# Kernel optimization log

Measured on AMD Instinct MI355X. Metric: run time of the kernel, lower is better.

## Reference

```python
import jax, jax.numpy as jnp
import numpy as np

B, D, T, NT, DS, G = 1024, 512, 36, 64, 32, 4
EPS = 1e-5


def setup_inputs() -> dict:
    key = jax.random.key(0)
    ks = jax.random.split(key, 8)
    return {
        "x": jax.random.normal(ks[0], (B, D, T, 1), jnp.float32),
        "y": jax.random.normal(ks[1], (B, D, T, 1), jnp.float32),
        "my_tokens": jax.random.normal(ks[2], (NT, D), jnp.float32) * 0.02,
        "gate": jax.random.normal(ks[3], (1,), jnp.float32) * 0.1,
        "gate_av": jax.random.normal(ks[4], (1,), jnp.float32) * 0.1,
        "w_down": jax.random.normal(ks[5], (DS, D // G), jnp.float32) * 0.05,  # Conv2d(512->32,1,groups=4) weight [32,128,1,1] squeezed
        "w_up": jax.random.normal(ks[6], (D, DS // G), jnp.float32) * 0.05,    # Conv2d(32->512,1,groups=4) weight [512,8,1,1] squeezed
        "bn1_g": jnp.ones((DS,), jnp.float32), "bn1_b": jnp.zeros((DS,), jnp.float32),
        "bn2_g": jnp.ones((D,), jnp.float32), "bn2_b": jnp.zeros((D,), jnp.float32),
        "lnb_g": jnp.ones((D,), jnp.float32), "lnb_b": jnp.zeros((D,), jnp.float32),
        "lnp_g": jnp.ones((D,), jnp.float32), "lnp_b": jnp.zeros((D,), jnp.float32),
    }


def _layernorm(h, g, b):  # normalize last dim
    mu = jnp.mean(h, axis=-1, keepdims=True)
    var = jnp.var(h, axis=-1, keepdims=True)
    return (h - mu) * jax.lax.rsqrt(var + EPS) * g + b


def _batchnorm(z, g, b):  # z: [B,C,T], training-mode batch stats over (B,T)
    mu = jnp.mean(z, axis=(0, 2), keepdims=True)
    var = jnp.var(z, axis=(0, 2), keepdims=True)
    return (z - mu) * jax.lax.rsqrt(var + EPS) * g[None, :, None] + b[None, :, None]


def reference(x, y, my_tokens, gate, gate_av, w_down, w_up,
              bn1_g, bn1_b, bn2_g, bn2_b, lnb_g, lnb_b, lnp_g, lnp_b):
    xs = x[..., 0]  # [B,D,T]
    ys = y[..., 0]  # [B,D,T]
    # token <- y cross attention
    att_y2tk = jax.nn.softmax(jnp.einsum('td,bds->bts', my_tokens, ys), axis=-1)  # [B,NT,T]
    rep = my_tokens[None] + jnp.einsum('bts,bds->btd', att_y2tk, ys)  # [B,NT,D]
    # x <- token cross attention
    att_tk2x = jax.nn.softmax(jnp.einsum('bds,btd->bst', xs, rep), axis=-1)  # [B,T,NT]
    x_res = jnp.einsum('bst,btd->bsd', att_tk2x, rep)  # [B,T,D]
    xc = xs + gate_av[0] * jnp.swapaxes(x_res, 1, 2)  # [B,D,T]
    # ln_before over channel dim
    h = jnp.swapaxes(_layernorm(jnp.swapaxes(xc, 1, 2), lnb_g, lnb_b), 1, 2)  # [B,D,T]
    # grouped 1x1 down conv
    hg = h.reshape(h.shape[0], G, D // G, T)
    z = jnp.einsum('bgct,goc->bgot', hg, w_down.reshape(G, DS // G, D // G)).reshape(h.shape[0], DS, T)
    z = jax.nn.relu(_batchnorm(z, bn1_g, bn1_b))
    # grouped 1x1 up conv
    zg = z.reshape(z.shape[0], G, DS // G, T)
    o = jnp.einsum('bgct,goc->bgot', zg, w_up.reshape(G, D // G, DS // G)).reshape(z.shape[0], D, T)
    o = _batchnorm(o, bn2_g, bn2_b)
    o = jnp.swapaxes(_layernorm(jnp.swapaxes(o, 1, 2), lnp_g, lnp_b), 1, 2)
    return (gate[0] * o)[..., None]  # [B,D,T,1]
```

## Files before the change

### kernel.cpp

```cpp
#include <hip/hip_runtime.h>

#define B_ 1024
#define D_ 512
#define T_ 36
#define NT_ 64
#define DS_ 32
#define EPS_ 1e-5f

typedef float f32x4 __attribute__((ext_vector_type(4)));
typedef __bf16 bf16x8 __attribute__((ext_vector_type(8)));
typedef unsigned short u16x8 __attribute__((ext_vector_type(8)));

#define DEVI static __device__ __forceinline__
#define MFMA16 __builtin_amdgcn_mfma_f32_16x16x32_bf16

DEVI unsigned short f2bf(float f) { return __builtin_bit_cast(unsigned short, (__bf16)f); }
DEVI float bf2f(unsigned short h) { return (float)__builtin_bit_cast(__bf16, h); }

DEVI unsigned swz(int row, int col) {
    return (unsigned)(row * 1024 + ((2 * col) ^ ((row & 7) << 4)));
}

#define OFF_XST 73728
#define OFF_SC  122880
#define OFF_A1  133632
#define OFF_A2  142848
#define OFF_GT  149760
#define K1_LDS  156672

__global__ __launch_bounds__(512)
void k0_prepack(const float* __restrict__ tok, const float* __restrict__ wd,
                unsigned short* __restrict__ tokbf, float* __restrict__ tokTf,
                unsigned short* __restrict__ wdd)
{
    int i = blockIdx.x * 512 + threadIdx.x;
    if (i < 32768) {
        tokbf[i] = f2bf(tok[i]);
    } else if (i < 65536) {
        int j = i - 32768; int d = j >> 6, t = j & 63;
        tokTf[j] = tok[t * 512 + d];
    } else if (i < 81920) {
        int j = i - 65536; int o = j >> 9, dd = j & 511;
        wdd[j] = ((dd >> 7) == (o >> 3)) ? f2bf(wd[o * 128 + (dd & 127)]) : (unsigned short)0;
    }
}

__global__ __launch_bounds__(1024, 4)
void k1_fused(const float* __restrict__ x, const float* __restrict__ y,
              const unsigned short* __restrict__ tokbf, const float* __restrict__ tokTf,
              const float* __restrict__ gav_p, const unsigned short* __restrict__ wdd,
              const float* __restrict__ lnbg, const float* __restrict__ lnbb,
              float* __restrict__ z_pre)
{
    extern __shared__ char lds[];
    float* sc = (float*)(lds + OFF_SC);
    unsigned short* a1 = (unsigned short*)(lds + OFF_A1);
    unsigned short* a2 = (unsigned short*)(lds + OFF_A2);
    unsigned short* gt = (unsigned short*)(lds + OFF_GT);

    const int b    = blockIdx.x;
    const int tid  = threadIdx.x;
    const int lane = tid & 63;
    const int w    = tid >> 6;
    const int l15  = lane & 15;
    const int l4   = lane >> 4;

    const float* yb = y + b * (D_ * T_);
    const float* xb = x + b * (D_ * T_);

    {
        unsigned* z1 = (unsigned*)(lds + 36 * 1024);
        unsigned* z2 = (unsigned*)(lds + OFF_XST + 36 * 1024);
        for (int i = tid; i < 3072; i += 1024) { z1[i] = 0u; z2[i] = 0u; }
        unsigned* z3 = (unsigned*)(lds + OFF_A1);
        for (int i = tid; i < 5760; i += 1024) z3[i] = 0u;
    }
    for (int ww = tid; ww < 1152; ww += 1024) {
        int isx = (ww >= 576) ? 1 : 0;
        int u = isx ? (ww - 576) : ww;
        const float* src = isx ? xb : yb;
        char* dst = lds + (isx ? OFF_XST : 0);
        int dblk = u / 9, s4 = u - dblk * 9;
        int s0 = s4 * 4;
        const float* bp = src + dblk * 8 * T_ + s0;
        u16x8 u0, u1, u2, u3;
        #pragma unroll
        for (int r = 0; r < 8; ++r) {
            f32x4 v = *(const f32x4*)(bp + r * T_);
            u0[r] = f2bf(v[0]); u1[r] = f2bf(v[1]);
            u2[r] = f2bf(v[2]); u3[r] = f2bf(v[3]);
        }
        *(u16x8*)(dst + swz(s0 + 0, dblk * 8)) = u0;
        *(u16x8*)(dst + swz(s0 + 1, dblk * 8)) = u1;
        *(u16x8*)(dst + swz(s0 + 2, dblk * 8)) = u2;
        *(u16x8*)(dst + swz(s0 + 3, dblk * 8)) = u3;
    }
    __syncthreads();

    for (int tile = w; tile < 21; tile += 16) {
        f32x4 acc0 = {0.f,0.f,0.f,0.f}, acc1 = {0.f,0.f,0.f,0.f};
        if (tile < 12) {
            int mt = tile / 3, nt = tile % 3;
            int trow = mt * 16 + l15, srow = nt * 16 + l15;
            #pragma unroll
            for (int ks = 0; ks < 16; ks += 2) {
                int ka = ks * 32 + l4 * 8, kb = ka + 32;
                acc0 = MFMA16(*(const bf16x8*)(tokbf + trow * 512 + ka),
                              *(const bf16x8*)(lds + swz(srow, ka)), acc0, 0, 0, 0);
                acc1 = MFMA16(*(const bf16x8*)(tokbf + trow * 512 + kb),
                              *(const bf16x8*)(lds + swz(srow, kb)), acc1, 0, 0, 0);
            }
            f32x4 acc = acc0 + acc1;
            if (srow < T_) {
                #pragma unroll
                for (int j = 0; j < 4; ++j)
                    sc[(mt * 16 + l4 * 4 + j) * 42 + srow] = acc[j];
            }
        } else {
            int g2 = tile - 12;
            int mt = g2 / 3, nt = g2 % 3;
            int arow = mt * 16 + l15, brow = nt * 16 + l15;
            #pragma unroll
            for (int ks = 0; ks < 16; ks += 2) {
                int ka = ks * 32 + l4 * 8, kb = ka + 32;
                acc0 = MFMA16(*(const bf16x8*)(lds + OFF_XST + swz(arow, ka)),
                              *(const bf16x8*)(lds + swz(brow, ka)), acc0, 0, 0, 0);
                acc1 = MFMA16(*(const bf16x8*)(lds + OFF_XST + swz(arow, kb)),
                              *(const bf16x8*)(lds + swz(brow, kb)), acc1, 0, 0, 0);
            }
            f32x4 acc = acc0 + acc1;
            if (brow < T_) {
                #pragma unroll
                for (int j = 0; j < 4; ++j) {
                    int gr = mt * 16 + l4 * 4 + j;
                    if (gr < T_) gt[gr * 72 + brow] = f2bf(acc[j]);
                }
            }
        }
    }
    __syncthreads();

    {
        int t = tid >> 4, l16 = tid & 15;
        const float* scp = sc + t * 42;
        float v0 = scp[l16];
        float v1 = scp[l16 + 16];
        float v2 = (l16 < 4) ? scp[l16 + 32] : -1e30f;
        float m = fmaxf(fmaxf(v0, v1), v2);
        #pragma unroll
        for (int off = 1; off < 16; off <<= 1) m = fmaxf(m, __shfl_xor(m, off));
        float e0 = __expf(v0 - m), e1 = __expf(v1 - m);
        float e2 = (l16 < 4) ? __expf(v2 - m) : 0.f;
        float ssum = e0 + e1 + e2;
        #pragma unroll
        for (int off = 1; off < 16; off <<= 1) ssum += __shfl_xor(ssum, off);
        float inv = 1.f / ssum;
        a1[t * 72 + l16]      = f2bf(e0 * inv);
        a1[t * 72 + l16 + 16] = f2bf(e1 * inv);
        if (l16 < 4) a1[t * 72 + l16 + 32] = f2bf(e2 * inv);
    }
    __syncthreads();

    #pragma unroll
    for (int i = 0; i < 8; ++i) {
        int q = w + 16 * i;
        int dt = q & 31, tt = q >> 5;
        int dbase = dt * 16, tbase = tt * 16;
        const float* yrow = yb + (dbase + l15) * T_;
        f32x4 p0 = *(const f32x4*)(yrow + l4 * 8);
        f32x4 p1 = *(const f32x4*)(yrow + l4 * 8 + 4);
        bf16x8 fa0, fa1;
        #pragma unroll
        for (int j = 0; j < 4; ++j) { fa0[j] = (__bf16)p0[j]; fa0[4 + j] = (__bf16)p1[j]; }
        if (l4 == 0) {
            f32x4 p2 = *(const f32x4*)(yrow + 32);
            #pragma unroll
            for (int j = 0; j < 4; ++j) { fa1[j] = (__bf16)p2[j]; fa1[4 + j] = (__bf16)0.f; }
        } else {
            #pragma unroll
            for (int j = 0; j < 8; ++j) fa1[j] = (__bf16)0.f;
        }
        bf16x8 fb0 = *(const bf16x8*)(a1 + (tbase + l15) * 72 + l4 * 8);
        bf16x8 fb1 = *(const bf16x8*)(a1 + (tbase + l15) * 72 + 32 + l4 * 8);
        f32x4 acc = {0.f,0.f,0.f,0.f};
        acc = MFMA16(fa0, fb0, acc, 0, 0, 0);
        acc = MFMA16(fa1, fb1, acc, 0, 0, 0);
        #pragma unroll
        for (int j = 0; j < 4; ++j) {
            int d = dbase + l4 * 4 + j;
            float val = tokTf[d * 64 + tbase + l15] + acc[j];
            *(unsigned short*)(lds + d * 144 + 2 * (tbase + l15)) = f2bf(val);
        }
    }
    if (w < 12) {
        int mt = w / 3, nt = w % 3;
        int trow = mt * 16 + l15, srow = nt * 16 + l15;
        f32x4 acc0 = {0.f,0.f,0.f,0.f}, acc1 = {0.f,0.f,0.f,0.f};
        #pragma unroll
        for (int ks = 0; ks < 16; ks += 2) {
            int ka = ks * 32 + l4 * 8, kb = ka + 32;
            acc0 = MFMA16(*(const bf16x8*)(tokbf + trow * 512 + ka),
                          *(const bf16x8*)(lds + OFF_XST + swz(srow, ka)), acc0, 0, 0, 0);
            acc1 = MFMA16(*(const bf16x8*)(tokbf + trow * 512 + kb),
                          *(const bf16x8*)(lds + OFF_XST + swz(srow, kb)), acc1, 0, 0, 0);
        }
        acc0 = MFMA16(*(const bf16x8*)(a1 + trow * 72 + l4 * 8),
                      *(const bf16x8*)(gt + srow * 72 + l4 * 8), acc0, 0, 0, 0);
        acc1 = MFMA16(*(const bf16x8*)(a1 + trow * 72 + 32 + l4 * 8),
                      *(const bf16x8*)(gt + srow * 72 + 32 + l4 * 8), acc1, 0, 0, 0);
        f32x4 acc = acc0 + acc1;
        if (srow < T_) {
            #pragma unroll
            for (int j = 0; j < 4; ++j)
                sc[(mt * 16 + l4 * 4 + j) * 42 + srow] = acc[j];
        }
    }
    __syncthreads();

    if (tid < 576) {
        int s = tid >> 4, l16 = tid & 15;
        float v0 = sc[(l16     ) * 42 + s];
        float v1 = sc[(l16 + 16) * 42 + s];
        float v2 = sc[(l16 + 32) * 42 + s];
        float v3 = sc[(l16 + 48) * 42 + s];
        float m = fmaxf(fmaxf(v0, v1), fmaxf(v2, v3));
        #pragma unroll
        for (int off = 1; off < 16; off <<= 1) m = fmaxf(m, __shfl_xor(m, off));
        float e0 = __expf(v0 - m), e1 = __expf(v1 - m), e2 = __expf(v2 - m), e3 = __expf(v3 - m);
        float ssum = e0 + e1 + e2 + e3;
        #pragma unroll
        for (int off = 1; off < 16; off <<= 1) ssum += __shfl_xor(ssum, off);
        float inv = 1.f / ssum;
        a2[s * 72 + l16]      = f2bf(e0 * inv);
        a2[s * 72 + l16 + 16] = f2bf(e1 * inv);
        a2[s * 72 + l16 + 32] = f2bf(e2 * inv);
        a2[s * 72 + l16 + 48] = f2bf(e3 * inv);
    }
    __syncthreads();

    {
        const float gav = gav_p[0];
        float* red = sc;
        f32x4 acc6[6];
        #pragma unroll
        for (int i = 0; i < 6; ++i) {
            int q = w * 6 + i;
            int dt = q & 31, st = q >> 5;
            int dbase = dt * 16, sbase = st * 16;
            f32x4 acc = {0.f,0.f,0.f,0.f};
            #pragma unroll
            for (int ks = 0; ks < 2; ++ks) {
                int k0 = ks * 32 + l4 * 8;
                bf16x8 af = *(const bf16x8*)(lds + (dbase + l15) * 144 + k0 * 2);
                bf16x8 bv = *(const bf16x8*)(a2 + (sbase + l15) * 72 + k0);
                acc = MFMA16(af, bv, acc, 0, 0, 0);
            }
            acc6[i] = acc;
        }
        #pragma unroll
        for (int i = 0; i < 6; ++i) {
            int q = w * 6 + i;
            int dt = q & 31, st = q >> 5;
            int dbase = dt * 16, sbase = st * 16;
            int s = sbase + l15;
            float rsum = 0.f, rsq = 0.f;
            if (s < T_) {
                #pragma unroll
                for (int j = 0; j < 4; ++j) {
                    int d = dbase + l4 * 4 + j;
                    float xsv = bf2f(*(const unsigned short*)(lds + OFF_XST + swz(s, d)));
                    float v = xsv + gav * acc6[i][j];
                    acc6[i][j] = v;
                    rsum += v; rsq += v * v;
                }
            }
            rsum += __shfl_xor(rsum, 16); rsq += __shfl_xor(rsq, 16);
            rsum += __shfl_xor(rsum, 32); rsq += __shfl_xor(rsq, 32);
            if (s < T_ && l4 == 0) {
                red[s * 32 + dt] = rsum;
                red[1152 + s * 32 + dt] = rsq;
            }
        }
        __syncthreads();
        if (tid < T_) {
            int s = tid; float S = 0.f, Q = 0.f;
            #pragma unroll
            for (int q = 0; q < 32; ++q) { S += red[s * 32 + q]; Q += red[1152 + s * 32 + q]; }
            float mu = S * (1.f / 512.f);
            float var = Q * (1.f / 512.f) - mu * mu;
            red[2304 + s] = mu; red[2340 + s] = rsqrtf(var + EPS_);
        }
        __syncthreads();
        #pragma unroll
        for (int i = 0; i < 6; ++i) {
            int q = w * 6 + i;
            int dt = q & 31, st = q >> 5;
            int dbase = dt * 16, sbase = st * 16;
            int s = sbase + l15;
            if (s < T_) {
                float mu = red[2304 + s], rsig = red[2340 + s];
                #pragma unroll
                for (int j = 0; j < 4; ++j) {
                    int d = dbase + l4 * 4 + j;
                    float g = lnbg[d], bb2 = lnbb[d];
                    *(unsigned short*)(lds + OFF_XST + swz(s, d)) =
                        f2bf((acc6[i][j] - mu) * rsig * g + bb2);
                }
            }
        }
    }
    __syncthreads();

    if (w < 6) {
        int mt = w / 3, nt = w % 3;
        int orow = mt * 16 + l15, srow = nt * 16 + l15;
        f32x4 acc0 = {0.f,0.f,0.f,0.f}, acc1 = {0.f,0.f,0.f,0.f};
        #pragma unroll
        for (int ks = 0; ks < 16; ks += 2) {
            int ka = ks * 32 + l4 * 8, kb = ka + 32;
            acc0 = MFMA16(*(const bf16x8*)(wdd + orow * 512 + ka),
                          *(const bf16x8*)(lds + OFF_XST + swz(srow, ka)), acc0, 0, 0, 0);
            acc1 = MFMA16(*(const bf16x8*)(wdd + orow * 512 + kb),
                          *(const bf16x8*)(lds + OFF_XST + swz(srow, kb)), acc1, 0, 0, 0);
        }
        f32x4 acc = acc0 + acc1;
        if (srow < T_) {
            #pragma unroll
            for (int j = 0; j < 4; ++j)
                z_pre[b * (DS_ * T_) + (mt * 16 + l4 * 4 + j) * T_ + srow] = acc[j];
        }
    }
}

__global__ __launch_bounds__(256)
void k3a_bn1part(const float* __restrict__ z_pre, float* __restrict__ p3)
{
    __shared__ float rbuf[4][2];
    int blk = blockIdx.x;
    int o = blk & 31, sl = blk >> 5;
    int tid = threadIdx.x;
    float S = 0.f, Q = 0.f;
    for (int i = tid; i < 64 * T_; i += 256) {
        int bb = sl * 64 + i / T_, t = i - (i / T_) * T_;
        float v = z_pre[bb * (DS_ * T_) + o * T_ + t];
        S += v; Q += v * v;
    }
    #pragma unroll
    for (int off = 1; off < 64; off <<= 1) { S += __shfl_xor(S, off); Q += __shfl_xor(Q, off); }
    int ww = tid >> 6;
    if ((tid & 63) == 0) { rbuf[ww][0] = S; rbuf[ww][1] = Q; }
    __syncthreads();
    if (tid == 0) {
        float s2 = 0.f, q2 = 0.f;
        for (int i = 0; i < 4; ++i) { s2 += rbuf[i][0]; q2 += rbuf[i][1]; }
        p3[blk * 2] = s2; p3[blk * 2 + 1] = q2;
    }
}

__global__ __launch_bounds__(64)
void k3b_bn1stats(const float* __restrict__ p3, float* __restrict__ st1)
{
    int o = threadIdx.x;
    if (o < 32) {
        float S = 0.f, Q = 0.f;
        for (int sl = 0; sl < 16; ++sl) {
            S += p3[((sl << 5) | o) * 2];
            Q += p3[((sl << 5) | o) * 2 + 1];
        }
        float mu = S / 36864.f;
        float var = Q / 36864.f - mu * mu;
        st1[o] = mu; st1[32 + o] = rsqrtf(var + EPS_);
    }
}

__global__ __launch_bounds__(256)
void k4m_moments(const float* __restrict__ z_pre, const float* __restrict__ st1,
                 const float* __restrict__ g1p, const float* __restrict__ b1p,
                 float* __restrict__ m4)
{
    __shared__ float zr[32][40];
    int blk = blockIdx.x, tid = threadIdx.x;
    int c2 = tid & 7, c1 = (tid >> 3) & 7, g = tid >> 6;
    int ch1 = g * 8 + c1, ch2 = g * 8 + c2;
    float acc = 0.f, asum = 0.f;
    for (int bi = 0; bi < 8; ++bi) {
        int b = blk * 8 + bi;
        __syncthreads();
        for (int i = tid; i < DS_ * T_; i += 256) {
            int o = i / T_, t = i - o * T_;
            float v = z_pre[b * (DS_ * T_) + i];
            zr[o][t] = fmaxf(0.f, (v - st1[o]) * st1[32 + o] * g1p[o] + b1p[o]);
        }
        __syncthreads();
        for (int t = 0; t < T_; ++t) {
            float a = zr[ch1][t], b2 = zr[ch2][t];
            acc += a * b2;
            asum += a;
        }
    }
    m4[blk * 288 + tid] = acc;
    if (c1 == c2) m4[blk * 288 + 256 + g * 8 + c1] = asum;
}

__global__ __launch_bounds__(512)
void k4s_bn2stats(const float* __restrict__ m4, const float* __restrict__ wu,
                  float* __restrict__ st2)
{
    __shared__ float M2[256], mz[32];
    int tid = threadIdx.x;
    if (tid < 256) {
        float S = 0.f;
        for (int k = 0; k < 128; ++k) S += m4[k * 288 + tid];
        M2[tid] = S * (1.f / 36864.f);
    } else if (tid < 288) {
        int j = tid - 256;
        float S = 0.f;
        for (int k = 0; k < 128; ++k) S += m4[k * 288 + 256 + j];
        mz[j] = S * (1.f / 36864.f);
    }
    __syncthreads();
    int d = tid, g = d >> 7;
    float wr[8];
    #pragma unroll
    for (int c = 0; c < 8; ++c) wr[c] = wu[d * 8 + c];
    float mu2 = 0.f;
    #pragma unroll
    for (int c = 0; c < 8; ++c) mu2 += wr[c] * mz[g * 8 + c];
    float e2 = 0.f;
    #pragma unroll
    for (int c = 0; c < 8; ++c)
        #pragma unroll
        for (int c2 = 0; c2 < 8; ++c2)
            e2 += wr[c] * wr[c2] * M2[g * 64 + c * 8 + c2];
    st2[d] = mu2;
    st2[512 + d] = rsqrtf(e2 - mu2 * mu2 + EPS_);
}

#define K5_LDS 47888
__global__ __launch_bounds__(512, 6)
void k5_final(const float* __restrict__ z_pre, const float* __restrict__ st1,
              const float* __restrict__ g1p, const float* __restrict__ b1p,
              const float* __restrict__ wu, const float* __restrict__ st2,
              const float* __restrict__ g2p, const float* __restrict__ b2p,
              const float* __restrict__ lnpg, const float* __restrict__ lnpb,
              const float* __restrict__ gate_p, float* __restrict__ out)
{
    extern __shared__ char lds[];
    unsigned short* o_f = (unsigned short*)lds;
    float* zrT = (float*)(lds + 41984);
    int b = blockIdx.x;
    int tid = threadIdx.x;

    for (int i = tid; i < DS_ * T_; i += 512) {
        int o = i / T_, s = i - o * T_;
        float v = z_pre[b * (DS_ * T_) + i];
        zrT[s * 41 + o] = fmaxf(0.f, (v - st1[o]) * st1[32 + o] * g1p[o] + b1p[o]);
    }
    __syncthreads();

    for (int i = tid; i < D_ * T_; i += 512) {
        int d = i / T_, t = i - d * T_;
        const float* zp = &zrT[t * 41 + (d >> 7) * 8];
        const float* wp = &wu[d * 8];
        f32x4 w0 = *(const f32x4*)wp;
        f32x4 w1 = *(const f32x4*)(wp + 4);
        float acc = zp[0]*w0[0] + zp[1]*w0[1] + zp[2]*w0[2] + zp[3]*w0[3]
                  + zp[4]*w1[0] + zp[5]*w1[1] + zp[6]*w1[2] + zp[7]*w1[3];
        o_f[d * 41 + t] = f2bf((acc - st2[d]) * st2[512 + d] * g2p[d] + b2p[d]);
    }
    __syncthreads();

    int w = tid >> 6, lane = tid & 63;
    float gate = gate_p[0];
    for (int t = w; t < T_; t += 8) {
        float S = 0.f, Q = 0.f;
        float v[8];
        #pragma unroll
        for (int i2 = 0; i2 < 8; ++i2) {
            float vv = bf2f(o_f[(i2 * 64 + lane) * 41 + t]);
            v[i2] = vv; S += vv; Q += vv * vv;
        }
        #pragma unroll
        for (int off = 1; off < 64; off <<= 1) { S += __shfl_xor(S, off); Q += __shfl_xor(Q, off); }
        float mu = S * (1.f / 512.f);
        float var = Q * (1.f / 512.f) - mu * mu;
        float rs = rsqrtf(var + EPS_);
        #pragma unroll
        for (int i2 = 0; i2 < 8; ++i2) {
            int d = i2 * 64 + lane;
            o_f[d * 41 + t] = f2bf(gate * ((v[i2] - mu) * rs * lnpg[d] + lnpb[d]));
        }
    }
    __syncthreads();

    float* ob = out + b * (D_ * T_);
    for (int i = tid; i < D_ * T_; i += 512) {
        int d = i / T_, t = i - d * T_;
        ob[i] = bf2f(o_f[d * 41 + t]);
    }
}

extern "C" void kernel_launch(void* const* d_in, const int* in_sizes, int n_in,
                              void* d_out, int out_size, void* d_ws, size_t ws_size,
                              hipStream_t stream)
{
    (void)in_sizes; (void)n_in; (void)out_size; (void)ws_size;
    const float* x    = (const float*)d_in[0];
    const float* y    = (const float*)d_in[1];
    const float* tok  = (const float*)d_in[2];
    const float* gate = (const float*)d_in[3];
    const float* gav  = (const float*)d_in[4];
    const float* wd   = (const float*)d_in[5];
    const float* wu   = (const float*)d_in[6];
    const float* bn1g = (const float*)d_in[7];
    const float* bn1b = (const float*)d_in[8];
    const float* bn2g = (const float*)d_in[9];
    const float* bn2b = (const float*)d_in[10];
    const float* lnbg = (const float*)d_in[11];
    const float* lnbb = (const float*)d_in[12];
    const float* lnpg = (const float*)d_in[13];
    const float* lnpb = (const float*)d_in[14];
    float* out = (float*)d_out;

    char* ws = (char*)d_ws;
    float* z_pre          = (float*)ws;
    float* st1            = (float*)(ws + 4718592);
    unsigned short* tokbf = (unsigned short*)(ws + 4719104);
    float* tokTf          = (float*)(ws + 4784640);
    unsigned short* wdd   = (unsigned short*)(ws + 4915712);
    float* p3             = (float*)(ws + 4948480);
    float* m4             = (float*)(ws + 4952576);
    float* st2            = (float*)(ws + 5100032);

    hipFuncSetAttribute((const void*)k1_fused, hipFuncAttributeMaxDynamicSharedMemorySize, K1_LDS);
    hipFuncSetAttribute((const void*)k5_final, hipFuncAttributeMaxDynamicSharedMemorySize, K5_LDS);

    k0_prepack<<<160, 512, 0, stream>>>(tok, wd, tokbf, tokTf, wdd);
    k1_fused<<<B_, 1024, K1_LDS, stream>>>(x, y, tokbf, tokTf, gav, wdd, lnbg, lnbb, z_pre);
    k3a_bn1part<<<512, 256, 0, stream>>>(z_pre, p3);
    k3b_bn1stats<<<1, 64, 0, stream>>>(p3, st1);
    k4m_moments<<<128, 256, 0, stream>>>(z_pre, st1, bn1g, bn1b, m4);
    k4s_bn2stats<<<1, 512, 0, stream>>>(m4, wu, st2);
    k5_final<<<B_, 512, K5_LDS, stream>>>(z_pre, st1, bn1g, bn1b, wu, st2, bn2g, bn2b,
                                          lnpg, lnpb, gate, out);
}
```

Baseline: 212.9 us.

## Stage y as bf16 in LDS and reuse A fragments across token tiles

```diff
diff --git a/kernel.cpp b/kernel.cpp
--- a/kernel.cpp
+++ b/kernel.cpp
@@ -10,6 +10,7 @@
 typedef float f32x4 __attribute__((ext_vector_type(4)));
 typedef __bf16 bf16x8 __attribute__((ext_vector_type(8)));
 typedef unsigned short u16x8 __attribute__((ext_vector_type(8)));
+typedef unsigned short u16x4 __attribute__((ext_vector_type(4)));
 
 #define DEVI static __device__ __forceinline__
 #define MFMA16 __builtin_amdgcn_mfma_f32_16x16x32_bf16
@@ -159,37 +160,51 @@
         a1[t * 72 + l16 + 16] = f2bf(e1 * inv);
         if (l16 < 4) a1[t * 72 + l16 + 32] = f2bf(e2 * inv);
     }
-    __syncthreads();
-
-    #pragma unroll
-    for (int i = 0; i < 8; ++i) {
-        int q = w + 16 * i;
-        int dt = q & 31, tt = q >> 5;
-        int dbase = dt * 16, tbase = tt * 16;
-        const float* yrow = yb + (dbase + l15) * T_;
-        f32x4 p0 = *(const f32x4*)(yrow + l4 * 8);
-        f32x4 p1 = *(const f32x4*)(yrow + l4 * 8 + 4);
-        bf16x8 fa0, fa1;
-        #pragma unroll
-        for (int j = 0; j < 4; ++j) { fa0[j] = (__bf16)p0[j]; fa0[4 + j] = (__bf16)p1[j]; }
-        if (l4 == 0) {
-            f32x4 p2 = *(const f32x4*)(yrow + 32);
-            #pragma unroll
-            for (int j = 0; j < 4; ++j) { fa1[j] = (__bf16)p2[j]; fa1[4 + j] = (__bf16)0.f; }
-        } else {
-            #pragma unroll
-            for (int j = 0; j < 8; ++j) fa1[j] = (__bf16)0.f;
-        }
-        bf16x8 fb0 = *(const bf16x8*)(a1 + (tbase + l15) * 72 + l4 * 8);
-        bf16x8 fb1 = *(const bf16x8*)(a1 + (tbase + l15) * 72 + 32 + l4 * 8);
-        f32x4 acc = {0.f,0.f,0.f,0.f};
-        acc = MFMA16(fa0, fb0, acc, 0, 0, 0);
-        acc = MFMA16(fa1, fb1, acc, 0, 0, 0);
-        #pragma unroll
-        for (int j = 0; j < 4; ++j) {
-            int d = dbase + l4 * 4 + j;
-            float val = tokTf[d * 64 + tbase + l15] + acc[j];
-            *(unsigned short*)(lds + d * 144 + 2 * (tbase + l15)) = f2bf(val);
+    for (int j = tid; j < 4608; j += 1024) {
+        int row = j / 9, q = j - row * 9;
+        f32x4 v = *(const f32x4*)(yb + row * 36 + q * 4);
+        u16x4 h;
+        #pragma unroll
+        for (int jj = 0; jj < 4; ++jj) h[jj] = f2bf(v[jj]);
+        *(u16x4*)(lds + row * 144 + q * 8) = h;
+    }
+    if (tid < 512) {
+        char* p = lds + tid * 144;
+        u16x4 z4 = {0,0,0,0}; u16x8 z8 = {0,0,0,0,0,0,0,0};
+        *(u16x4*)(p + 72) = z4;
+        *(u16x8*)(p + 80) = z8;
+        *(u16x8*)(p + 96) = z8;
+        *(u16x8*)(p + 112) = z8;
+    }
+    __syncthreads();
+
+    {
+        #pragma unroll
+        for (int half = 0; half < 2; ++half) {
+            int dbase = (w + 16 * half) * 16;
+            bf16x8 fa0 = *(const bf16x8*)(lds + (dbase + l15) * 144 + l4 * 16);
+            bf16x8 fa1 = *(const bf16x8*)(lds + (dbase + l15) * 144 + 64 + l4 * 16);
+            f32x4 c[4];
+            #pragma unroll
+            for (int tt = 0; tt < 4; ++tt) {
+                int tbase = tt * 16;
+                bf16x8 fb0 = *(const bf16x8*)(a1 + (tbase + l15) * 72 + l4 * 8);
+                bf16x8 fb1 = *(const bf16x8*)(a1 + (tbase + l15) * 72 + 32 + l4 * 8);
+                f32x4 acc = {0.f,0.f,0.f,0.f};
+                acc = MFMA16(fa0, fb0, acc, 0, 0, 0);
+                acc = MFMA16(fa1, fb1, acc, 0, 0, 0);
+                c[tt] = acc;
+            }
+            #pragma unroll
+            for (int tt = 0; tt < 4; ++tt) {
+                int tbase = tt * 16;
+                #pragma unroll
+                for (int j = 0; j < 4; ++j) {
+                    int d = dbase + l4 * 4 + j;
+                    float val = tokTf[d * 64 + tbase + l15] + c[tt][j];
+                    *(unsigned short*)(lds + d * 144 + 2 * (tbase + l15)) = f2bf(val);
+                }
+            }
         }
     }
     if (w < 12) {
@@ -277,18 +292,18 @@
             rsum += __shfl_xor(rsum, 16); rsq += __shfl_xor(rsq, 16);
             rsum += __shfl_xor(rsum, 32); rsq += __shfl_xor(rsq, 32);
             if (s < T_ && l4 == 0) {
-                red[s * 32 + dt] = rsum;
-                red[1152 + s * 32 + dt] = rsq;
+                red[dt * 40 + s] = rsum;
+                red[1280 + dt * 40 + s] = rsq;
             }
         }
         __syncthreads();
         if (tid < T_) {
             int s = tid; float S = 0.f, Q = 0.f;
             #pragma unroll
-            for (int q = 0; q < 32; ++q) { S += red[s * 32 + q]; Q += red[1152 + s * 32 + q]; }
+            for (int q = 0; q < 32; ++q) { S += red[q * 40 + s]; Q += red[1280 + q * 40 + s]; }
             float mu = S * (1.f / 512.f);
             float var = Q * (1.f / 512.f) - mu * mu;
-            red[2304 + s] = mu; red[2340 + s] = rsqrtf(var + EPS_);
+            red[2560 + s] = mu; red[2600 + s] = rsqrtf(var + EPS_);
         }
         __syncthreads();
         #pragma unroll
@@ -298,7 +313,7 @@
             int dbase = dt * 16, sbase = st * 16;
             int s = sbase + l15;
             if (s < T_) {
-                float mu = red[2304 + s], rsig = red[2340 + s];
+                float mu = red[2560 + s], rsig = red[2600 + s];
                 #pragma unroll
                 for (int j = 0; j < 4; ++j) {
                     int d = dbase + l4 * 4 + j;
```

Result: faster. 200.0 us (-6.1%).

## Split x transpose into separate kernel and reassociate rep computation to shrink LDS

Applied to the files above, without the earlier changes.

```diff
diff --git a/kernel.cpp b/kernel.cpp
--- a/kernel.cpp
+++ b/kernel.cpp
@@ -10,6 +10,7 @@
 typedef float f32x4 __attribute__((ext_vector_type(4)));
 typedef __bf16 bf16x8 __attribute__((ext_vector_type(8)));
 typedef unsigned short u16x8 __attribute__((ext_vector_type(8)));
+typedef unsigned short u16x4 __attribute__((ext_vector_type(4)));
 
 #define DEVI static __device__ __forceinline__
 #define MFMA16 __builtin_amdgcn_mfma_f32_16x16x32_bf16
@@ -21,16 +22,16 @@
     return (unsigned)(row * 1024 + ((2 * col) ^ ((row & 7) << 4)));
 }
 
-#define OFF_XST 73728
-#define OFF_SC  122880
-#define OFF_A1  133632
-#define OFF_A2  142848
-#define OFF_GT  149760
-#define K1_LDS  156672
+#define LDS_A2  40960
+#define LDS_SC  49152
+#define LDS_A1  58624
+#define LDS_A1T 67840
+#define LDS_GT  74752
+#define K1_LDS  81664
 
 __global__ __launch_bounds__(512)
 void k0_prepack(const float* __restrict__ tok, const float* __restrict__ wd,
-                unsigned short* __restrict__ tokbf, float* __restrict__ tokTf,
+                unsigned short* __restrict__ tokbf, unsigned short* __restrict__ tokT,
                 unsigned short* __restrict__ wdd)
 {
     int i = blockIdx.x * 512 + threadIdx.x;
@@ -38,27 +39,63 @@
         tokbf[i] = f2bf(tok[i]);
     } else if (i < 65536) {
         int j = i - 32768; int d = j >> 6, t = j & 63;
-        tokTf[j] = tok[t * 512 + d];
+        tokT[j] = f2bf(tok[t * 512 + d]);
     } else if (i < 81920) {
         int j = i - 65536; int o = j >> 9, dd = j & 511;
         wdd[j] = ((dd >> 7) == (o >> 3)) ? f2bf(wd[o * 128 + (dd & 127)]) : (unsigned short)0;
     }
 }
 
-__global__ __launch_bounds__(1024, 4)
-void k1_fused(const float* __restrict__ x, const float* __restrict__ y,
-              const unsigned short* __restrict__ tokbf, const float* __restrict__ tokTf,
+__global__ __launch_bounds__(512)
+void kA_xpose(const float* __restrict__ x, unsigned short* __restrict__ xT, int b0)
+{
+    __shared__ char sl[49152];
+    const int b = b0 + blockIdx.x;
+    const int tid = threadIdx.x;
+    const float* xb = x + b * (D_ * T_);
+    unsigned short* xTb = xT + (size_t)blockIdx.x * 24576;
+
+    for (int u = tid; u < 576; u += 512) {
+        int dblk = u / 9, s4 = u - dblk * 9;
+        int s0 = s4 * 4;
+        const float* bp = xb + dblk * 8 * T_ + s0;
+        u16x8 u0, u1, u2, u3;
+        #pragma unroll
+        for (int r = 0; r < 8; ++r) {
+            f32x4 v = *(const f32x4*)(bp + r * T_);
+            u0[r] = f2bf(v[0]); u1[r] = f2bf(v[1]);
+            u2[r] = f2bf(v[2]); u3[r] = f2bf(v[3]);
+        }
+        *(u16x8*)(sl + swz(s0 + 0, dblk * 8)) = u0;
+        *(u16x8*)(sl + swz(s0 + 1, dblk * 8)) = u1;
+        *(u16x8*)(sl + swz(s0 + 2, dblk * 8)) = u2;
+        *(u16x8*)(sl + swz(s0 + 3, dblk * 8)) = u3;
+    }
+    __syncthreads();
+    for (int i = tid; i < 2304; i += 512) {
+        int row = i >> 6, l = i & 63;
+        *(u16x8*)(xTb + row * 512 + l * 8) = *(const u16x8*)(sl + swz(row, l * 8));
+    }
+    for (int i = tid; i < 3072; i += 512)
+        ((unsigned*)(xTb + 36 * 512))[i] = 0u;
+}
+
+__global__ __launch_bounds__(512, 4)
+void k1_fused(const unsigned short* __restrict__ xT, const float* __restrict__ y,
+              const unsigned short* __restrict__ tokbf, const unsigned short* __restrict__ tokT,
               const float* __restrict__ gav_p, const unsigned short* __restrict__ wdd,
               const float* __restrict__ lnbg, const float* __restrict__ lnbb,
-              float* __restrict__ z_pre)
+              float* __restrict__ z_pre, int b0)
 {
     extern __shared__ char lds[];
-    float* sc = (float*)(lds + OFF_SC);
-    unsigned short* a1 = (unsigned short*)(lds + OFF_A1);
-    unsigned short* a2 = (unsigned short*)(lds + OFF_A2);
-    unsigned short* gt = (unsigned short*)(lds + OFF_GT);
-
-    const int b    = blockIdx.x;
+    float* sc = (float*)(lds + LDS_SC);
+    unsigned short* a1  = (unsigned short*)(lds + LDS_A1);
+    unsigned short* a1t = (unsigned short*)(lds + LDS_A1T);
+    unsigned short* gt  = (unsigned short*)(lds + LDS_GT);
+    unsigned short* wb  = gt;
+    unsigned short* a2  = (unsigned short*)(lds + LDS_A2);
+
+    const int b    = b0 + blockIdx.x;
     const int tid  = threadIdx.x;
     const int lane = tid & 63;
     const int w    = tid >> 6;
@@ -66,23 +103,18 @@
     const int l4   = lane >> 4;
 
     const float* yb = y + b * (D_ * T_);
-    const float* xb = x + b * (D_ * T_);
+    const unsigned short* xTb = xT + (size_t)blockIdx.x * 24576;
 
     {
         unsigned* z1 = (unsigned*)(lds + 36 * 1024);
-        unsigned* z2 = (unsigned*)(lds + OFF_XST + 36 * 1024);
-        for (int i = tid; i < 3072; i += 1024) { z1[i] = 0u; z2[i] = 0u; }
-        unsigned* z3 = (unsigned*)(lds + OFF_A1);
-        for (int i = tid; i < 5760; i += 1024) z3[i] = 0u;
-    }
-    for (int ww = tid; ww < 1152; ww += 1024) {
-        int isx = (ww >= 576) ? 1 : 0;
-        int u = isx ? (ww - 576) : ww;
-        const float* src = isx ? xb : yb;
-        char* dst = lds + (isx ? OFF_XST : 0);
+        for (int i = tid; i < 3072; i += 512) z1[i] = 0u;
+        unsigned* z3 = (unsigned*)(lds + LDS_A1);
+        for (int i = tid; i < 5760; i += 512) z3[i] = 0u;
+    }
+    for (int u = tid; u < 576; u += 512) {
         int dblk = u / 9, s4 = u - dblk * 9;
         int s0 = s4 * 4;
-        const float* bp = src + dblk * 8 * T_ + s0;
+        const float* bp = yb + dblk * 8 * T_ + s0;
         u16x8 u0, u1, u2, u3;
         #pragma unroll
         for (int r = 0; r < 8; ++r) {
@@ -90,17 +122,17 @@
             u0[r] = f2bf(v[0]); u1[r] = f2bf(v[1]);
             u2[r] = f2bf(v[2]); u3[r] = f2bf(v[3]);
         }
-        *(u16x8*)(dst + swz(s0 + 0, dblk * 8)) = u0;
-        *(u16x8*)(dst + swz(s0 + 1, dblk * 8)) = u1;
-        *(u16x8*)(dst + swz(s0 + 2, dblk * 8)) = u2;
-        *(u16x8*)(dst + swz(s0 + 3, dblk * 8)) = u3;
-    }
-    __syncthreads();
-
-    for (int tile = w; tile < 21; tile += 16) {
+        *(u16x8*)(lds + swz(s0 + 0, dblk * 8)) = u0;
+        *(u16x8*)(lds + swz(s0 + 1, dblk * 8)) = u1;
+        *(u16x8*)(lds + swz(s0 + 2, dblk * 8)) = u2;
+        *(u16x8*)(lds + swz(s0 + 3, dblk * 8)) = u3;
+    }
+    __syncthreads();
+
+    for (int tl = w; tl < 21; tl += 8) {
         f32x4 acc0 = {0.f,0.f,0.f,0.f}, acc1 = {0.f,0.f,0.f,0.f};
-        if (tile < 12) {
-            int mt = tile / 3, nt = tile % 3;
+        if (tl < 12) {
+            int mt = tl / 3, nt = tl % 3;
             int trow = mt * 16 + l15, srow = nt * 16 + l15;
             #pragma unroll
             for (int ks = 0; ks < 16; ks += 2) {
@@ -114,95 +146,79 @@
             if (srow < T_) {
                 #pragma unroll
                 for (int j = 0; j < 4; ++j)
-                    sc[(mt * 16 + l4 * 4 + j) * 42 + srow] = acc[j];
+                    sc[(mt * 16 + l4 * 4 + j) * 37 + srow] = acc[j];
             }
         } else {
-            int g2 = tile - 12;
+            int g2 = tl - 12;
             int mt = g2 / 3, nt = g2 % 3;
             int arow = mt * 16 + l15, brow = nt * 16 + l15;
             #pragma unroll
             for (int ks = 0; ks < 16; ks += 2) {
                 int ka = ks * 32 + l4 * 8, kb = ka + 32;
-                acc0 = MFMA16(*(const bf16x8*)(lds + OFF_XST + swz(arow, ka)),
+                acc0 = MFMA16(*(const bf16x8*)(xTb + arow * 512 + ka),
                               *(const bf16x8*)(lds + swz(brow, ka)), acc0, 0, 0, 0);
-                acc1 = MFMA16(*(const bf16x8*)(lds + OFF_XST + swz(arow, kb)),
+                acc1 = MFMA16(*(const bf16x8*)(xTb + arow * 512 + kb),
                               *(const bf16x8*)(lds + swz(brow, kb)), acc1, 0, 0, 0);
             }
             f32x4 acc = acc0 + acc1;
-            if (brow < T_) {
-                #pragma unroll
-                for (int j = 0; j < 4; ++j) {
-                    int gr = mt * 16 + l4 * 4 + j;
-                    if (gr < T_) gt[gr * 72 + brow] = f2bf(acc[j]);
-                }
-            }
+            #pragma unroll
+            for (int j = 0; j < 4; ++j)
+                gt[(mt * 16 + l4 * 4 + j) * 72 + brow] = f2bf(acc[j]);
         }
     }
     __syncthreads();
 
     {
-        int t = tid >> 4, l16 = tid & 15;
-        const float* scp = sc + t * 42;
-        float v0 = scp[l16];
-        float v1 = scp[l16 + 16];
-        float v2 = (l16 < 4) ? scp[l16 + 32] : -1e30f;
-        float m = fmaxf(fmaxf(v0, v1), v2);
-        #pragma unroll
-        for (int off = 1; off < 16; off <<= 1) m = fmaxf(m, __shfl_xor(m, off));
-        float e0 = __expf(v0 - m), e1 = __expf(v1 - m);
-        float e2 = (l16 < 4) ? __expf(v2 - m) : 0.f;
-        float ssum = e0 + e1 + e2;
-        #pragma unroll
-        for (int off = 1; off < 16; off <<= 1) ssum += __shfl_xor(ssum, off);
+        int t = tid >> 3, l8 = tid & 7;
+        const float* scp = sc + t * 37;
+        float v0 = scp[l8], v1 = scp[l8 + 8], v2 = scp[l8 + 16], v3 = scp[l8 + 24];
+        float v4 = (l8 < 4) ? scp[l8 + 32] : -1e30f;
+        float m = fmaxf(fmaxf(fmaxf(v0, v1), fmaxf(v2, v3)), v4);
+        #pragma unroll
+        for (int off = 1; off < 8; off <<= 1) m = fmaxf(m, __shfl_xor(m, off));
+        float e0 = __expf(v0 - m), e1 = __expf(v1 - m), e2 = __expf(v2 - m), e3 = __expf(v3 - m);
+        float e4 = (l8 < 4) ? __expf(v4 - m) : 0.f;
+        float ssum = e0 + e1 + e2 + e3 + e4;
+        #pragma unroll
+        for (int off = 1; off < 8; off <<= 1) ssum += __shfl_xor(ssum, off);
         float inv = 1.f / ssum;
-        a1[t * 72 + l16]      = f2bf(e0 * inv);
-        a1[t * 72 + l16 + 16] = f2bf(e1 * inv);
-        if (l16 < 4) a1[t * 72 + l16 + 32] = f2bf(e2 * inv);
-    }
-    __syncthreads();
-
-    #pragma unroll
-    for (int i = 0; i < 8; ++i) {
-        int q = w + 16 * i;
-        int dt = q & 31, tt = q >> 5;
-        int dbase = dt * 16, tbase = tt * 16;
-        const float* yrow = yb + (dbase + l15) * T_;
-        f32x4 p0 = *(const f32x4*)(yrow + l4 * 8);
-        f32x4 p1 = *(const f32x4*)(yrow + l4 * 8 + 4);
-        bf16x8 fa0, fa1;
-        #pragma unroll
-        for (int j = 0; j < 4; ++j) { fa0[j] = (__bf16)p0[j]; fa0[4 + j] = (__bf16)p1[j]; }
-        if (l4 == 0) {
-            f32x4 p2 = *(const f32x4*)(yrow + 32);
-            #pragma unroll
-            for (int j = 0; j < 4; ++j) { fa1[j] = (__bf16)p2[j]; fa1[4 + j] = (__bf16)0.f; }
-        } else {
-            #pragma unroll
-            for (int j = 0; j < 8; ++j) fa1[j] = (__bf16)0.f;
-        }
-        bf16x8 fb0 = *(const bf16x8*)(a1 + (tbase + l15) * 72 + l4 * 8);
-        bf16x8 fb1 = *(const bf16x8*)(a1 + (tbase + l15) * 72 + 32 + l4 * 8);
-        f32x4 acc = {0.f,0.f,0.f,0.f};
-        acc = MFMA16(fa0, fb0, acc, 0, 0, 0);
-        acc = MFMA16(fa1, fb1, acc, 0, 0, 0);
-        #pragma unroll
-        for (int j = 0; j < 4; ++j) {
-            int d = dbase + l4 * 4 + j;
-            float val = tokTf[d * 64 + tbase + l15] + acc[j];
-            *(unsigned short*)(lds + d * 144 + 2 * (tbase + l15)) = f2bf(val);
-        }
-    }
-    if (w < 12) {
-        int mt = w / 3, nt = w % 3;
+        unsigned short h0 = f2bf(e0 * inv), h1 = f2bf(e1 * inv);
+        unsigned short h2 = f2bf(e2 * inv), h3 = f2bf(e3 * inv);
+        a1[t * 72 + l8]      = h0;  a1t[l8 * 72 + t]        = h0;
+        a1[t * 72 + l8 + 8]  = h1;  a1t[(l8 + 8) * 72 + t]  = h1;
+        a1[t * 72 + l8 + 16] = h2;  a1t[(l8 + 16) * 72 + t] = h2;
+        a1[t * 72 + l8 + 24] = h3;  a1t[(l8 + 24) * 72 + t] = h3;
+        if (l8 < 4) {
+            unsigned short h4 = f2bf(e4 * inv);
+            a1[t * 72 + l8 + 32] = h4;
+            a1t[(l8 + 32) * 72 + t] = h4;
+        }
+    }
+    for (int j = tid; j < 4608; j += 512) {
+        int row = j / 9, q = j - row * 9;
+        f32x4 v = *(const f32x4*)(yb + row * T_ + q * 4);
+        u16x4 hh;
+        #pragma unroll
+        for (int jj = 0; jj < 4; ++jj) hh[jj] = f2bf(v[jj]);
+        *(u16x4*)(lds + row * 80 + q * 8) = hh;
+    }
+    {
+        u16x4 z4 = {0, 0, 0, 0};
+        *(u16x4*)(lds + tid * 80 + 72) = z4;
+    }
+    __syncthreads();
+
+    for (int tl = w; tl < 12; tl += 8) {
+        int mt = tl / 3, nt = tl % 3;
         int trow = mt * 16 + l15, srow = nt * 16 + l15;
         f32x4 acc0 = {0.f,0.f,0.f,0.f}, acc1 = {0.f,0.f,0.f,0.f};
         #pragma unroll
         for (int ks = 0; ks < 16; ks += 2) {
             int ka = ks * 32 + l4 * 8, kb = ka + 32;
             acc0 = MFMA16(*(const bf16x8*)(tokbf + trow * 512 + ka),
-                          *(const bf16x8*)(lds + OFF_XST + swz(srow, ka)), acc0, 0, 0, 0);
+                          *(const bf16x8*)(xTb + srow * 512 + ka), acc0, 0, 0, 0);
             acc1 = MFMA16(*(const bf16x8*)(tokbf + trow * 512 + kb),
-                          *(const bf16x8*)(lds + OFF_XST + swz(srow, kb)), acc1, 0, 0, 0);
+                          *(const bf16x8*)(xTb + srow * 512 + kb), acc1, 0, 0, 0);
         }
         acc0 = MFMA16(*(const bf16x8*)(a1 + trow * 72 + l4 * 8),
                       *(const bf16x8*)(gt + srow * 72 + l4 * 8), acc0, 0, 0, 0);
@@ -212,99 +228,120 @@
         if (srow < T_) {
             #pragma unroll
             for (int j = 0; j < 4; ++j)
-                sc[(mt * 16 + l4 * 4 + j) * 42 + srow] = acc[j];
-        }
-    }
-    __syncthreads();
-
-    if (tid < 576) {
-        int s = tid >> 4, l16 = tid & 15;
-        float v0 = sc[(l16     ) * 42 + s];
-        float v1 = sc[(l16 + 16) * 42 + s];
-        float v2 = sc[(l16 + 32) * 42 + s];
-        float v3 = sc[(l16 + 48) * 42 + s];
-        float m = fmaxf(fmaxf(v0, v1), fmaxf(v2, v3));
-        #pragma unroll
-        for (int off = 1; off < 16; off <<= 1) m = fmaxf(m, __shfl_xor(m, off));
-        float e0 = __expf(v0 - m), e1 = __expf(v1 - m), e2 = __expf(v2 - m), e3 = __expf(v3 - m);
-        float ssum = e0 + e1 + e2 + e3;
-        #pragma unroll
-        for (int off = 1; off < 16; off <<= 1) ssum += __shfl_xor(ssum, off);
+                sc[(mt * 16 + l4 * 4 + j) * 37 + srow] = acc[j];
+        }
+    }
+    __syncthreads();
+
+    if ((tid >> 3) < T_) {
+        int s = tid >> 3, l8 = tid & 7;
+        float v[8];
+        #pragma unroll
+        for (int k = 0; k < 8; ++k) v[k] = sc[(l8 + 8 * k) * 37 + s];
+        float m = v[0];
+        #pragma unroll
+        for (int k = 1; k < 8; ++k) m = fmaxf(m, v[k]);
+        #pragma unroll
+        for (int off = 1; off < 8; off <<= 1) m = fmaxf(m, __shfl_xor(m, off));
+        float e[8], ssum = 0.f;
+        #pragma unroll
+        for (int k = 0; k < 8; ++k) { e[k] = __expf(v[k] - m); ssum += e[k]; }
+        #pragma unroll
+        for (int off = 1; off < 8; off <<= 1) ssum += __shfl_xor(ssum, off);
         float inv = 1.f / ssum;
-        a2[s * 72 + l16]      = f2bf(e0 * inv);
-        a2[s * 72 + l16 + 16] = f2bf(e1 * inv);
-        a2[s * 72 + l16 + 32] = f2bf(e2 * inv);
-        a2[s * 72 + l16 + 48] = f2bf(e3 * inv);
+        #pragma unroll
+        for (int k = 0; k < 8; ++k) a2[s * 72 + l8 + 8 * k] = f2bf(e[k] * inv);
+    }
+    __syncthreads();
+
+    for (int tl = w; tl < 9; tl += 8) {
+        int mt = tl / 3, nt = tl % 3;
+        f32x4 acc = {0.f,0.f,0.f,0.f};
+        #pragma unroll
+        for (int ks = 0; ks < 2; ++ks) {
+            int k0 = ks * 32 + l4 * 8;
+            acc = MFMA16(*(const bf16x8*)(a2 + (mt * 16 + l15) * 72 + k0),
+                         *(const bf16x8*)(a1t + (nt * 16 + l15) * 72 + k0), acc, 0, 0, 0);
+        }
+        #pragma unroll
+        for (int j = 0; j < 4; ++j)
+            wb[(mt * 16 + l4 * 4 + j) * 72 + nt * 16 + l15] = f2bf(acc[j]);
     }
     __syncthreads();
 
     {
         const float gav = gav_p[0];
         float* red = sc;
-        f32x4 acc6[6];
-        #pragma unroll
-        for (int i = 0; i < 6; ++i) {
-            int q = w * 6 + i;
-            int dt = q & 31, st = q >> 5;
-            int dbase = dt * 16, sbase = st * 16;
-            f32x4 acc = {0.f,0.f,0.f,0.f};
-            #pragma unroll
-            for (int ks = 0; ks < 2; ++ks) {
-                int k0 = ks * 32 + l4 * 8;
-                bf16x8 af = *(const bf16x8*)(lds + (dbase + l15) * 144 + k0 * 2);
-                bf16x8 bv = *(const bf16x8*)(a2 + (sbase + l15) * 72 + k0);
-                acc = MFMA16(af, bv, acc, 0, 0, 0);
-            }
-            acc6[i] = acc;
-        }
-        #pragma unroll
-        for (int i = 0; i < 6; ++i) {
-            int q = w * 6 + i;
-            int dt = q & 31, st = q >> 5;
-            int dbase = dt * 16, sbase = st * 16;
-            int s = sbase + l15;
-            float rsum = 0.f, rsq = 0.f;
+        f32x4 acc[3][4];
+        #pragma unroll
+        for (int st = 0; st < 3; ++st) {
+            int sbase = st * 16;
+            bf16x8 b10 = *(const bf16x8*)(a2 + (sbase + l15) * 72 + l4 * 8);
+            bf16x8 b11 = *(const bf16x8*)(a2 + (sbase + l15) * 72 + 32 + l4 * 8);
+            bf16x8 b20 = *(const bf16x8*)(wb + (sbase + l15) * 72 + l4 * 8);
+            bf16x8 b21 = *(const bf16x8*)(wb + (sbase + l15) * 72 + 32 + l4 * 8);
+            #pragma unroll
+            for (int dt = 0; dt < 4; ++dt) {
+                int drow = (w * 4 + dt) * 16 + l15;
+                bf16x8 a10 = *(const bf16x8*)(tokT + drow * 64 + l4 * 8);
+                bf16x8 a11 = *(const bf16x8*)(tokT + drow * 64 + 32 + l4 * 8);
+                bf16x8 a20 = *(const bf16x8*)(lds + drow * 80 + l4 * 16);
+                bf16x8 a21 = *(const bf16x8*)(lds + drow * 80 + 64 + l4 * 16);
+                f32x4 a = {0.f,0.f,0.f,0.f};
+                a = MFMA16(a10, b10, a, 0, 0, 0);
+                a = MFMA16(a11, b11, a, 0, 0, 0);
+                a = MFMA16(a20, b20, a, 0, 0, 0);
+                a = MFMA16(a21, b21, a, 0, 0, 0);
+                acc[st][dt] = a;
+            }
+        }
+        float rs_[3] = {0.f,0.f,0.f}, rq_[3] = {0.f,0.f,0.f};
+        #pragma unroll
+        for (int st = 0; st < 3; ++st) {
+            int s = st * 16 + l15;
             if (s < T_) {
                 #pragma unroll
-                for (int j = 0; j < 4; ++j) {
-                    int d = dbase + l4 * 4 + j;
-                    float xsv = bf2f(*(const unsigned short*)(lds + OFF_XST + swz(s, d)));
-                    float v = xsv + gav * acc6[i][j];
-                    acc6[i][j] = v;
-                    rsum += v; rsq += v * v;
+                for (int dt = 0; dt < 4; ++dt) {
+                    #pragma unroll
+                    for (int j = 0; j < 4; ++j) {
+                        int d = (w * 4 + dt) * 16 + l4 * 4 + j;
+                        float xsv = bf2f(xTb[s * 512 + d]);
+                        float v = xsv + gav * acc[st][dt][j];
+                        acc[st][dt][j] = v;
+                        rs_[st] += v; rq_[st] += v * v;
+                    }
                 }
             }
-            rsum += __shfl_xor(rsum, 16); rsq += __shfl_xor(rsq, 16);
-            rsum += __shfl_xor(rsum, 32); rsq += __shfl_xor(rsq, 32);
+            rs_[st] += __shfl_xor(rs_[st], 16); rq_[st] += __shfl_xor(rq_[st], 16);
+            rs_[st] += __shfl_xor(rs_[st], 32); rq_[st] += __shfl_xor(rq_[st], 32);
             if (s < T_ && l4 == 0) {
-                red[s * 32 + dt] = rsum;
-                red[1152 + s * 32 + dt] = rsq;
+                red[w * 40 + s] = rs_[st];
+                red[320 + w * 40 + s] = rq_[st];
             }
         }
         __syncthreads();
         if (tid < T_) {
-            int s = tid; float S = 0.f, Q = 0.f;
-            #pragma unroll
-            for (int q = 0; q < 32; ++q) { S += red[s * 32 + q]; Q += red[1152 + s * 32 + q]; }
+            float S = 0.f, Q = 0.f;
+            #pragma unroll
+            for (int q = 0; q < 8; ++q) { S += red[q * 40 + tid]; Q += red[320 + q * 40 + tid]; }
             float mu = S * (1.f / 512.f);
             float var = Q * (1.f / 512.f) - mu * mu;
-            red[2304 + s] = mu; red[2340 + s] = rsqrtf(var + EPS_);
+            red[640 + tid] = mu; red[680 + tid] = rsqrtf(var + EPS_);
         }
         __syncthreads();
         #pragma unroll
-        for (int i = 0; i < 6; ++i) {
-            int q = w * 6 + i;
-            int dt = q & 31, st = q >> 5;
-            int dbase = dt * 16, sbase = st * 16;
-            int s = sbase + l15;
+        for (int st = 0; st < 3; ++st) {
+            int s = st * 16 + l15;
             if (s < T_) {
-                float mu = red[2304 + s], rsig = red[2340 + s];
+                float mu = red[640 + s], rsg = red[680 + s];
                 #pragma unroll
-                for (int j = 0; j < 4; ++j) {
-                    int d = dbase + l4 * 4 + j;
-                    float g = lnbg[d], bb2 = lnbb[d];
-                    *(unsigned short*)(lds + OFF_XST + swz(s, d)) =
-                        f2bf((acc6[i][j] - mu) * rsig * g + bb2);
+                for (int dt = 0; dt < 4; ++dt) {
+                    #pragma unroll
+                    for (int j = 0; j < 4; ++j) {
+                        int d = (w * 4 + dt) * 16 + l4 * 4 + j;
+                        *(unsigned short*)(lds + swz(s, d)) =
+                            f2bf((acc[st][dt][j] - mu) * rsg * lnbg[d] + lnbb[d]);
+                    }
                 }
             }
         }
@@ -319,9 +356,9 @@
         for (int ks = 0; ks < 16; ks += 2) {
             int ka = ks * 32 + l4 * 8, kb = ka + 32;
             acc0 = MFMA16(*(const bf16x8*)(wdd + orow * 512 + ka),
-                          *(const bf16x8*)(lds + OFF_XST + swz(srow, ka)), acc0, 0, 0, 0);
+                          *(const bf16x8*)(lds + swz(srow, ka)), acc0, 0, 0, 0);
             acc1 = MFMA16(*(const bf16x8*)(wdd + orow * 512 + kb),
-                          *(const bf16x8*)(lds + OFF_XST + swz(srow, kb)), acc1, 0, 0, 0);
+                          *(const bf16x8*)(lds + swz(srow, kb)), acc1, 0, 0, 0);
         }
         f32x4 acc = acc0 + acc1;
         if (srow < T_) {
@@ -504,7 +541,7 @@
                               void* d_out, int out_size, void* d_ws, size_t ws_size,
                               hipStream_t stream)
 {
-    (void)in_sizes; (void)n_in; (void)out_size; (void)ws_size;
+    (void)in_sizes; (void)n_in; (void)out_size;
     const float* x    = (const float*)d_in[0];
     const float* y    = (const float*)d_in[1];
     const float* tok  = (const float*)d_in[2];
@@ -526,17 +563,27 @@
     float* z_pre          = (float*)ws;
     float* st1            = (float*)(ws + 4718592);
     unsigned short* tokbf = (unsigned short*)(ws + 4719104);
-    float* tokTf          = (float*)(ws + 4784640);
-    unsigned short* wdd   = (unsigned short*)(ws + 4915712);
-    float* p3             = (float*)(ws + 4948480);
-    float* m4             = (float*)(ws + 4952576);
-    float* st2            = (float*)(ws + 5100032);
+    unsigned short* tokT  = (unsigned short*)(ws + 4784640);
+    unsigned short* wdd   = (unsigned short*)(ws + 4850176);
+    float* p3             = (float*)(ws + 4882944);
+    float* m4             = (float*)(ws + 4887040);
+    float* st2            = (float*)(ws + 5034496);
+    unsigned short* xT    = (unsigned short*)(ws + 5038592);
+
+    size_t avail = (ws_size > 5038592) ? (ws_size - 5038592) : 49152;
+    int chunk = (int)(avail / 49152);
+    if (chunk < 1) chunk = 1;
+    if (chunk > B_) chunk = B_;
 
     hipFuncSetAttribute((const void*)k1_fused, hipFuncAttributeMaxDynamicSharedMemorySize, K1_LDS);
     hipFuncSetAttribute((const void*)k5_final, hipFuncAttributeMaxDynamicSharedMemorySize, K5_LDS);
 
-    k0_prepack<<<160, 512, 0, stream>>>(tok, wd, tokbf, tokTf, wdd);
-    k1_fused<<<B_, 1024, K1_LDS, stream>>>(x, y, tokbf, tokTf, gav, wdd, lnbg, lnbb, z_pre);
+    k0_prepack<<<160, 512, 0, stream>>>(tok, wd, tokbf, tokT, wdd);
+    for (int b0 = 0; b0 < B_; b0 += chunk) {
+        int cnt = (b0 + chunk <= B_) ? chunk : (B_ - b0);
+        kA_xpose<<<cnt, 512, 0, stream>>>(x, xT, b0);
+        k1_fused<<<cnt, 512, K1_LDS, stream>>>(xT, y, tokbf, tokT, gav, wdd, lnbg, lnbb, z_pre, b0);
+    }
     k3a_bn1part<<<512, 256, 0, stream>>>(z_pre, p3);
     k3b_bn1stats<<<1, 64, 0, stream>>>(p3, st1);
     k4m_moments<<<128, 256, 0, stream>>>(z_pre, st1, bn1g, bn1b, m4);
```

Result: slower. 245.4 us (+15.3%).
